# Kernel optimization log

Measured on AMD Instinct MI355X. Metric: run time of the kernel, lower is better.

The kernel has to match this reference:

```python
import jax, jax.numpy as jnp
import numpy as np

B, N, F_, H, K_IN, K = 2, 768, 128, 128, 2, 2
TAU = 0.66


def setup_inputs() -> dict:
    key = jax.random.key(0)
    ks = jax.random.split(key, 8)
    s = lambda fan: 1.0 / np.sqrt(fan)
    X = jax.random.normal(ks[0], (B, N, F_), jnp.float32)
    # edge_feat RezeroMLP: Linear(F,H) -> act -> Linear(H,H)
    ef_w1 = jax.random.normal(ks[1], (F_, H), jnp.float32) * s(F_)
    ef_b1 = jnp.zeros((H,), jnp.float32)
    ef_w2 = jax.random.normal(ks[2], (H, H), jnp.float32) * s(H)
    ef_b2 = jnp.zeros((H,), jnp.float32)
    # rezero gate (init 0 in module; use small nonzero so the branch is exercised)
    gate = jnp.asarray(0.1, jnp.float32)
    # score_mlp RezeroMLP: Linear(k_in,H) -> ReLU -> Linear(H,k)
    sm_w1 = jax.random.normal(ks[3], (K_IN, H), jnp.float32) * s(K_IN)
    sm_b1 = jnp.zeros((H,), jnp.float32)
    sm_w2 = jax.random.normal(ks[4], (H, K), jnp.float32) * s(H)
    sm_b2 = jnp.zeros((K,), jnp.float32)
    # pre-sampled standard Gumbel noise for gumbel_softmax
    u = jax.random.uniform(ks[5], (B, N, N, K), jnp.float32, minval=1e-6, maxval=1.0 - 1e-6)
    gumbel = -jnp.log(-jnp.log(u))
    return {"X": X, "ef_w1": ef_w1, "ef_b1": ef_b1, "ef_w2": ef_w2, "ef_b2": ef_b2,
            "gate": gate, "sm_w1": sm_w1, "sm_b1": sm_b1, "sm_w2": sm_w2, "sm_b2": sm_b2,
            "gumbel": gumbel}


def reference(X, ef_w1, ef_b1, ef_w2, ef_b2, gate, sm_w1, sm_b1, sm_w2, sm_b2, gumbel):
    # edge_feat MLP: [B,N,F] -> [B,N,H]
    feats = jax.nn.relu(X @ ef_w1 + ef_b1) @ ef_w2 + ef_b2
    D = H // K_IN
    Xact = feats.reshape(B, N, D, K_IN)
    Xskip = X.reshape(B, N, D, K_IN)  # feat_dim == hidden_dim, proj is None
    Xc = (Xskip + gate * Xact).transpose(0, 3, 1, 2)  # [B,k_in,N,D]
    # pairwise outer product ('prod' scoring): [B,N,N,k_in]
    prod = jnp.einsum('bkid,bkjd->bijk', Xc, Xc)
    # per-edge score MLP: k_in -> H -> k
    scores = jax.nn.relu(prod @ sm_w1 + sm_b1) @ sm_w2 + sm_b2  # [B,N,N,k]
    logits = scores - jnp.max(scores, axis=-1, keepdims=True)
    # gumbel-softmax, hard (straight-through)
    y_soft = jax.nn.softmax((logits + gumbel) / TAU, axis=-1)
    y_hard = jax.nn.one_hot(jnp.argmax(y_soft, axis=-1), K, dtype=y_soft.dtype)
    y = y_hard + y_soft - jax.lax.stop_gradient(y_soft)
    # A = y @ zo with zo = [0,1,...]: probability/one-hot mass of 'edge' states
    zo = jnp.ones((K,), y.dtype).at[0].set(0.0)
    A = y @ zo  # [B,N,N]
    # zero diagonal and symmetrize via upper triangle
    Au = jnp.triu(A, 1)
    return Au + jnp.swapaxes(Au, -1, -2)
```

## Files before the change

### kernel.cpp

```cpp
#include <hip/hip_runtime.h>

#define BB 2
#define NN 768
#define FF 128
#define HH 128
#define TS 32
#define LST 68
#define NT (NN / TS)
#define NPAIR (NT * (NT + 1) / 2)
#define EROWS 2
#define THR 4e-3f

__device__ __forceinline__
double edge_exact_f64(const double* __restrict__ Xc, const double* __restrict__ wpack,
                      int b, int i, int j, double init) {
    const double* xi0 = Xc + ((size_t)(b * 2 + 0) * NN + i) * 64;
    const double* xj0 = Xc + ((size_t)(b * 2 + 0) * NN + j) * 64;
    const double* xi1 = Xc + ((size_t)(b * 2 + 1) * NN + i) * 64;
    const double* xj1 = Xc + ((size_t)(b * 2 + 1) * NN + j) * 64;
    double p0 = 0.0, p1 = 0.0;
#pragma unroll 4
    for (int d2 = 0; d2 < 32; ++d2) {
        double2 a0 = *(const double2*)&xi0[2 * d2];
        double2 b0 = *(const double2*)&xj0[2 * d2];
        double2 a1 = *(const double2*)&xi1[2 * d2];
        double2 b1 = *(const double2*)&xj1[2 * d2];
        p0 = fma(a0.y, b0.y, fma(a0.x, b0.x, p0));
        p1 = fma(a1.y, b1.y, fma(a1.x, b1.x, p1));
    }
    double m = init;
#pragma unroll 8
    for (int c = 0; c < HH; ++c) {
        double2 wab = *(const double2*)&wpack[4 * c];
        double2 wbw = *(const double2*)&wpack[4 * c + 2];
        double tt = fma(p1, wab.y, fma(p0, wab.x, wbw.x));
        tt = fmax(tt, 0.0);
        m = fma(tt, wbw.y, m);
    }
    return m;
}

__global__ __launch_bounds__(256)
void edgefeat_kernel(const float* __restrict__ X,
                     const float* __restrict__ w1, const float* __restrict__ b1,
                     const float* __restrict__ w2, const float* __restrict__ b2,
                     const float* __restrict__ gatep,
                     const float* __restrict__ sm_w1, const float* __restrict__ sm_b1,
                     const float* __restrict__ sm_w2,
                     double* __restrict__ Xc, float* __restrict__ Xcf,
                     double* __restrict__ wpack, float4* __restrict__ wpackf) {
    __shared__ float  Xs[EROWS][FF];
    __shared__ double Hp[2][EROWS][HH];
    __shared__ double Hs[EROWS][HH];
    const int tid = threadIdx.x;
    const int h  = tid & 127;
    const int kh = tid >> 7;
    const int row0 = blockIdx.x * EROWS;
    Xs[kh][h] = X[(size_t)(row0 + kh) * FF + h];
    if (blockIdx.x == 0 && kh == 0) {
        double a  = (double)sm_w1[h];
        double bq = (double)sm_w1[HH + h];
        double be = (double)sm_b1[h];
        double wd = (double)sm_w2[2 * h + 1] - (double)sm_w2[2 * h + 0];
        wpack[4 * h + 0] = a;  wpack[4 * h + 1] = bq;
        wpack[4 * h + 2] = be; wpack[4 * h + 3] = wd;
        wpackf[h] = make_float4((float)a, (float)bq, (float)be, (float)wd);
    }
    __syncthreads();
    const int f0 = kh * 64;
    double acc0 = (kh == 0) ? (double)b1[h] : 0.0;
    double acc1 = acc0;
    for (int f = f0; f < f0 + 64; ++f) {
        double w = (double)w1[f * HH + h];
        acc0 = fma((double)Xs[0][f], w, acc0);
        acc1 = fma((double)Xs[1][f], w, acc1);
    }
    Hp[kh][0][h] = acc0; Hp[kh][1][h] = acc1;
    __syncthreads();
    if (kh == 0) {
        double v0 = Hp[0][0][h] + Hp[1][0][h];
        double v1 = Hp[0][1][h] + Hp[1][1][h];
        Hs[0][h] = v0 > 0.0 ? v0 : 0.0;
        Hs[1][h] = v1 > 0.0 ? v1 : 0.0;
    }
    __syncthreads();
    acc0 = (kh == 0) ? (double)b2[h] : 0.0;
    acc1 = acc0;
    for (int c = f0; c < f0 + 64; ++c) {
        double w = (double)w2[c * HH + h];
        acc0 = fma(Hs[0][c], w, acc0);
        acc1 = fma(Hs[1][c], w, acc1);
    }
    Hp[kh][0][h] = acc0; Hp[kh][1][h] = acc1;
    __syncthreads();
    if (kh == 0) {
        const double gate = (double)gatep[0];
        const int k = h & 1, d = h >> 1;
        const int b = row0 / NN;
        const int i0 = row0 % NN;
#pragma unroll
        for (int r = 0; r < EROWS; ++r) {
            double a = Hp[0][r][h] + Hp[1][r][h];
            double v = (double)Xs[r][h] + gate * a;
            size_t idx = (((size_t)(b * 2 + k)) * NN + (i0 + r)) * 64 + d;
            Xc[idx]  = v;
            Xcf[idx] = (float)v;
        }
    }
}

__global__ __launch_bounds__(512, 6)
void edge_decide_kernel(const double* __restrict__ Xc,
                        const float* __restrict__ Xcf,
                        const double* __restrict__ wpack,
                        const float4* __restrict__ wpackf,
                        const float* __restrict__ sm_b2,
                        const float* __restrict__ gumbel,
                        float* __restrict__ out) {
    __shared__ float  Ai[2][TS][LST];
    __shared__ float  Aj[2][TS][LST];
    __shared__ float  As[TS][TS + 1];
    const int b = blockIdx.y;
    const int t = blockIdx.x;
    int ti = (int)((49.0 - sqrt(2401.0 - 8.0 * (double)t)) * 0.5);
    int base = ti * (49 - ti) / 2;
    if (t < base) { --ti; base = ti * (49 - ti) / 2; }
    else { int nb = (ti + 1) * (48 - ti) / 2; if (t >= nb) { ++ti; base = nb; } }
    const int tj = t - base + ti;
    const int tid = threadIdx.x;
    const int i0 = ti * TS, j0 = tj * TS;

    for (int q = 0; q < 2; ++q) {
        int flat = tid + 512 * q;
        int d4 = flat & 15;
        int r  = (flat >> 4) & 31;
        int k  = flat >> 9;
        size_t rowbase = ((size_t)(b * 2 + k)) * NN;
        *(float4*)&Ai[k][r][4 * d4] = *(const float4*)&Xcf[(rowbase + i0 + r) * 64 + 4 * d4];
        *(float4*)&Aj[k][r][4 * d4] = *(const float4*)&Xcf[(rowbase + j0 + r) * 64 + 4 * d4];
    }

    const int s  = tid & 1;
    const int e  = tid >> 1;
    const int rh = e >> 4;
    const int ch = e & 15;
    const int r0 = rh, r1 = rh + 16;
    const int c0 = 2 * ch, c1 = c0 + 1;
    const int lr  = (s == 0) ? r0 : r1;
    const int gr  = i0 + lr;
    const int gj0 = j0 + c0, gj1 = j0 + c1;

    float4 gv = *(const float4*)&gumbel[(((size_t)b * NN + gr) * NN + gj0) * 2];
    __syncthreads();

    float p000 = 0.f, p001 = 0.f, p010 = 0.f, p011 = 0.f;
    float p100 = 0.f, p101 = 0.f, p110 = 0.f, p111 = 0.f;
#pragma unroll
    for (int it = 0; it < 8; ++it) {
        const int d4 = (s + 2 * it) * 4;
        float4 a00 = *(const float4*)&Ai[0][r0][d4];
        float4 a01 = *(const float4*)&Ai[0][r1][d4];
        float4 a10 = *(const float4*)&Ai[1][r0][d4];
        float4 a11 = *(const float4*)&Ai[1][r1][d4];
        float4 b00 = *(const float4*)&Aj[0][c0][d4];
        float4 b01 = *(const float4*)&Aj[0][c1][d4];
        float4 b10 = *(const float4*)&Aj[1][c0][d4];
        float4 b11 = *(const float4*)&Aj[1][c1][d4];
        p000 = fmaf(a00.w, b00.w, fmaf(a00.z, b00.z, fmaf(a00.y, b00.y, fmaf(a00.x, b00.x, p000))));
        p001 = fmaf(a00.w, b01.w, fmaf(a00.z, b01.z, fmaf(a00.y, b01.y, fmaf(a00.x, b01.x, p001))));
        p010 = fmaf(a01.w, b00.w, fmaf(a01.z, b00.z, fmaf(a01.y, b00.y, fmaf(a01.x, b00.x, p010))));
        p011 = fmaf(a01.w, b01.w, fmaf(a01.z, b01.z, fmaf(a01.y, b01.y, fmaf(a01.x, b01.x, p011))));
        p100 = fmaf(a10.w, b10.w, fmaf(a10.z, b10.z, fmaf(a10.y, b10.y, fmaf(a10.x, b10.x, p100))));
        p101 = fmaf(a10.w, b11.w, fmaf(a10.z, b11.z, fmaf(a10.y, b11.y, fmaf(a10.x, b11.x, p101))));
        p110 = fmaf(a11.w, b10.w, fmaf(a11.z, b10.z, fmaf(a11.y, b10.y, fmaf(a11.x, b10.x, p110))));
        p111 = fmaf(a11.w, b11.w, fmaf(a11.z, b11.z, fmaf(a11.y, b11.y, fmaf(a11.x, b11.x, p111))));
    }
    p000 += __shfl_xor(p000, 1); p001 += __shfl_xor(p001, 1);
    p010 += __shfl_xor(p010, 1); p011 += __shfl_xor(p011, 1);
    p100 += __shfl_xor(p100, 1); p101 += __shfl_xor(p101, 1);
    p110 += __shfl_xor(p110, 1); p111 += __shfl_xor(p111, 1);

    const float pa0 = (s == 0) ? p000 : p010;
    const float pa1 = (s == 0) ? p100 : p110;
    const float pb0 = (s == 0) ? p001 : p011;
    const float pb1 = (s == 0) ? p101 : p111;

    float ma = 0.f, mb = 0.f;
    float4 wA[8], wB[8];
#pragma unroll
    for (int u = 0; u < 8; ++u) wA[u] = wpackf[u];
#pragma unroll 1
    for (int cg = 0; cg < 8; ++cg) {
        const float4* nxt1 = wpackf + (16 * cg + 8);
#pragma unroll
        for (int u = 0; u < 8; ++u) wB[u] = nxt1[u];
#pragma unroll
        for (int u = 0; u < 8; ++u) {
            float tt;
            tt = fmaf(pa1, wA[u].y, fmaf(pa0, wA[u].x, wA[u].z)); tt = fmaxf(tt, 0.f); ma = fmaf(tt, wA[u].w, ma);
            tt = fmaf(pb1, wA[u].y, fmaf(pb0, wA[u].x, wA[u].z)); tt = fmaxf(tt, 0.f); mb = fmaf(tt, wA[u].w, mb);
        }
        const float4* nxt2 = wpackf + ((cg < 7) ? (16 * cg + 16) : 0);
#pragma unroll
        for (int u = 0; u < 8; ++u) wA[u] = nxt2[u];
#pragma unroll
        for (int u = 0; u < 8; ++u) {
            float tt;
            tt = fmaf(pa1, wB[u].y, fmaf(pa0, wB[u].x, wB[u].z)); tt = fmaxf(tt, 0.f); ma = fmaf(tt, wB[u].w, ma);
            tt = fmaf(pb1, wB[u].y, fmaf(pb0, wB[u].x, wB[u].z)); tt = fmaxf(tt, 0.f); mb = fmaf(tt, wB[u].w, mb);
        }
    }

    const double bd = (double)sm_b2[1] - (double)sm_b2[0];
    double ia = bd + ((double)gv.y - (double)gv.x);
    double ib = bd + ((double)gv.w - (double)gv.z);
    float fa = ma + (float)ia;
    float fb = mb + (float)ib;
    float Aa = fa > 0.f ? 1.f : 0.f;
    float Ab = fb > 0.f ? 1.f : 0.f;
    if (__builtin_expect(fminf(fabsf(fa), fabsf(fb)) < THR, 0)) {
        if (fabsf(fa) < THR) Aa = edge_exact_f64(Xc, wpack, b, gr, gj0, ia) > 0.0 ? 1.f : 0.f;
        if (fabsf(fb) < THR) Ab = edge_exact_f64(Xc, wpack, b, gr, gj1, ib) > 0.0 ? 1.f : 0.f;
    }
    As[lr][c0] = Aa; As[lr][c1] = Ab;
    __syncthreads();

    if (ti != tj) {
        *(float2*)&out[((size_t)b * NN + gr) * NN + gj0] = make_float2(Aa, Ab);
        float2 tv = make_float2(As[c0][lr], As[c1][lr]);
        *(float2*)&out[((size_t)b * NN + j0 + lr) * NN + i0 + c0] = tv;
    } else {
        float v0 = (lr < c0) ? Aa : ((lr > c0) ? As[c0][lr] : 0.0f);
        float v1 = (lr < c1) ? Ab : ((lr > c1) ? As[c1][lr] : 0.0f);
        *(float2*)&out[((size_t)b * NN + gr) * NN + gj0] = make_float2(v0, v1);
    }
}

extern "C" void kernel_launch(void* const* d_in, const int* in_sizes, int n_in,
                              void* d_out, int out_size, void* d_ws, size_t ws_size,
                              hipStream_t stream) {
    const float* X      = (const float*)d_in[0];
    const float* ef_w1  = (const float*)d_in[1];
    const float* ef_b1  = (const float*)d_in[2];
    const float* ef_w2  = (const float*)d_in[3];
    const float* ef_b2  = (const float*)d_in[4];
    const float* gate   = (const float*)d_in[5];
    const float* sm_w1  = (const float*)d_in[6];
    const float* sm_b1  = (const float*)d_in[7];
    const float* sm_w2  = (const float*)d_in[8];
    const float* sm_b2  = (const float*)d_in[9];
    const float* gumbel = (const float*)d_in[10];
    float* out = (float*)d_out;

    double* Xc     = (double*)d_ws;
    double* wpack  = Xc + (size_t)BB * 2 * NN * 64;
    float4* wpackf = (float4*)(wpack + 4 * HH);
    float*  Xcf    = (float*)(wpackf + HH);

    edgefeat_kernel<<<BB * NN / EROWS, 256, 0, stream>>>(
        X, ef_w1, ef_b1, ef_w2, ef_b2, gate, sm_w1, sm_b1, sm_w2, Xc, Xcf, wpack, wpackf);
    dim3 grid(NPAIR, BB);
    edge_decide_kernel<<<grid, 512, 0, stream>>>(Xc, Xcf, wpack, wpackf, sm_b2, gumbel, out);
}
```

Before: 116.8 us.

## Replace per-edge score MLP with angular lookup table when biases are zero

```diff
diff --git a/kernel.cpp b/kernel.cpp
--- a/kernel.cpp
+++ b/kernel.cpp
@@ -10,6 +10,8 @@
 #define NPAIR (NT * (NT + 1) / 2)
 #define EROWS 2
 #define THR 4e-3f
+#define NBIN 8192
+#define PIf 3.14159265358979323846f
 
 __device__ __forceinline__
 double edge_exact_f64(const double* __restrict__ Xc, const double* __restrict__ wpack,
@@ -48,7 +50,8 @@
                      const float* __restrict__ sm_w1, const float* __restrict__ sm_b1,
                      const float* __restrict__ sm_w2,
                      double* __restrict__ Xc, float* __restrict__ Xcf,
-                     double* __restrict__ wpack, float4* __restrict__ wpackf) {
+                     double* __restrict__ wpack, float4* __restrict__ wpackf,
+                     float4* __restrict__ tab, float* __restrict__ flagp) {
     __shared__ float  Xs[EROWS][FF];
     __shared__ double Hp[2][EROWS][HH];
     __shared__ double Hs[EROWS][HH];
@@ -107,6 +110,38 @@
             Xcf[idx] = (float)v;
         }
     }
+
+    const int bin = blockIdx.x * 256 + tid;
+    if (bin < NBIN) {
+        const float D = 2.f * PIf / (float)NBIN;
+        float thL = -PIf + (float)bin * D, thR = thL + D;
+        float sL, cL, sR, cR;
+        sincosf(thL, &sL, &cL);
+        sincosf(thR, &sR, &cR);
+        float A = 0.f, Bv = 0.f, xa = 0.f, xb = 0.f, xw = 0.f;
+        int ncr = 0;
+#pragma unroll 8
+        for (int c = 0; c < HH; ++c) {
+            float a  = sm_w1[c], bq = sm_w1[HH + c];
+            float wd = sm_w2[2 * c + 1] - sm_w2[2 * c];
+            float hL = fmaf(a, cL, bq * sL);
+            float hR = fmaf(a, cR, bq * sR);
+            bool actL = hL > 0.f;
+            if (actL) { A = fmaf(wd, a, A); Bv = fmaf(wd, bq, Bv); }
+            if (actL != (hR > 0.f)) {
+                ++ncr;
+                float sg = actL ? -1.f : 1.f;
+                xa = sg * a; xb = sg * bq; xw = wd;
+            }
+        }
+        tab[2 * bin]     = make_float4(A, Bv, xa, xb);
+        tab[2 * bin + 1] = make_float4(xw, (ncr >= 2) ? 1.f : 0.f, 0.f, 0.f);
+        if (bin == 0) {
+            float fl = 0.f;
+            for (int c = 0; c < HH; ++c) if (sm_b1[c] != 0.f) fl = 1.f;
+            flagp[0] = fl;
+        }
+    }
 }
 
 __global__ __launch_bounds__(512, 6)
@@ -114,6 +149,7 @@
                         const float* __restrict__ Xcf,
                         const double* __restrict__ wpack,
                         const float4* __restrict__ wpackf,
+                        const float4* __restrict__ tab, const float* __restrict__ flagp,
                         const float* __restrict__ sm_b2,
                         const float* __restrict__ gumbel,
                         float* __restrict__ out) {
@@ -151,6 +187,7 @@
     const int gj0 = j0 + c0, gj1 = j0 + c1;
 
     float4 gv = *(const float4*)&gumbel[(((size_t)b * NN + gr) * NN + gj0) * 2];
+    const float biased = flagp[0];
     __syncthreads();
 
     float p000 = 0.f, p001 = 0.f, p010 = 0.f, p011 = 0.f;
@@ -185,29 +222,33 @@
     const float pb0 = (s == 0) ? p001 : p011;
     const float pb1 = (s == 0) ? p101 : p111;
 
-    float ma = 0.f, mb = 0.f;
-    float4 wA[8], wB[8];
+    float ma, mb;
+    bool xfa = false, xfb = false;
+    if (biased == 0.f) {
+        const float BS = (float)NBIN / (2.f * PIf);
+        float tha = atan2f(pa1, pa0);
+        float thb = atan2f(pb1, pb0);
+        int bina = (int)fminf(fmaxf((tha + PIf) * BS, 0.f), (float)(NBIN - 1));
+        int binb = (int)fminf(fmaxf((thb + PIf) * BS, 0.f), (float)(NBIN - 1));
+        float4 ta0 = tab[2 * bina], ta1 = tab[2 * bina + 1];
+        float4 tb0 = tab[2 * binb], tb1 = tab[2 * binb + 1];
+        ma = fmaf(ta0.x, pa0, ta0.y * pa1) + ta1.x * fmaxf(fmaf(ta0.z, pa0, ta0.w * pa1), 0.f);
+        mb = fmaf(tb0.x, pb0, tb0.y * pb1) + tb1.x * fmaxf(fmaf(tb0.z, pb0, tb0.w * pb1), 0.f);
+        xfa = (ta1.y != 0.f);
+        xfb = (tb1.y != 0.f);
+    } else {
+        ma = 0.f; mb = 0.f;
+#pragma unroll 1
+        for (int c = 0; c < HH; c += 8) {
+            float4 w[8];
 #pragma unroll
-    for (int u = 0; u < 8; ++u) wA[u] = wpackf[u];
-#pragma unroll 1
-    for (int cg = 0; cg < 8; ++cg) {
-        const float4* nxt1 = wpackf + (16 * cg + 8);
+            for (int u = 0; u < 8; ++u) w[u] = wpackf[c + u];
 #pragma unroll
-        for (int u = 0; u < 8; ++u) wB[u] = nxt1[u];
-#pragma unroll
-        for (int u = 0; u < 8; ++u) {
-            float tt;
-            tt = fmaf(pa1, wA[u].y, fmaf(pa0, wA[u].x, wA[u].z)); tt = fmaxf(tt, 0.f); ma = fmaf(tt, wA[u].w, ma);
-            tt = fmaf(pb1, wA[u].y, fmaf(pb0, wA[u].x, wA[u].z)); tt = fmaxf(tt, 0.f); mb = fmaf(tt, wA[u].w, mb);
-        }
-        const float4* nxt2 = wpackf + ((cg < 7) ? (16 * cg + 16) : 0);
-#pragma unroll
-        for (int u = 0; u < 8; ++u) wA[u] = nxt2[u];
-#pragma unroll
-        for (int u = 0; u < 8; ++u) {
-            float tt;
-            tt = fmaf(pa1, wB[u].y, fmaf(pa0, wB[u].x, wB[u].z)); tt = fmaxf(tt, 0.f); ma = fmaf(tt, wB[u].w, ma);
-            tt = fmaf(pb1, wB[u].y, fmaf(pb0, wB[u].x, wB[u].z)); tt = fmaxf(tt, 0.f); mb = fmaf(tt, wB[u].w, mb);
+            for (int u = 0; u < 8; ++u) {
+                float tt;
+                tt = fmaf(pa1, w[u].y, fmaf(pa0, w[u].x, w[u].z)); tt = fmaxf(tt, 0.f); ma = fmaf(tt, w[u].w, ma);
+                tt = fmaf(pb1, w[u].y, fmaf(pb0, w[u].x, w[u].z)); tt = fmaxf(tt, 0.f); mb = fmaf(tt, w[u].w, mb);
+            }
         }
     }
 
@@ -218,9 +259,9 @@
     float fb = mb + (float)ib;
     float Aa = fa > 0.f ? 1.f : 0.f;
     float Ab = fb > 0.f ? 1.f : 0.f;
-    if (__builtin_expect(fminf(fabsf(fa), fabsf(fb)) < THR, 0)) {
-        if (fabsf(fa) < THR) Aa = edge_exact_f64(Xc, wpack, b, gr, gj0, ia) > 0.0 ? 1.f : 0.f;
-        if (fabsf(fb) < THR) Ab = edge_exact_f64(Xc, wpack, b, gr, gj1, ib) > 0.0 ? 1.f : 0.f;
+    if (__builtin_expect(xfa || xfb || fminf(fabsf(fa), fabsf(fb)) < THR, 0)) {
+        if (xfa || fabsf(fa) < THR) Aa = edge_exact_f64(Xc, wpack, b, gr, gj0, ia) > 0.0 ? 1.f : 0.f;
+        if (xfb || fabsf(fb) < THR) Ab = edge_exact_f64(Xc, wpack, b, gr, gj1, ib) > 0.0 ? 1.f : 0.f;
     }
     As[lr][c0] = Aa; As[lr][c1] = Ab;
     __syncthreads();
@@ -256,9 +297,13 @@
     double* wpack  = Xc + (size_t)BB * 2 * NN * 64;
     float4* wpackf = (float4*)(wpack + 4 * HH);
     float*  Xcf    = (float*)(wpackf + HH);
+    float4* tab    = (float4*)(Xcf + (size_t)BB * 2 * NN * 64);
+    float*  flagp  = (float*)(tab + 2 * NBIN);
 
     edgefeat_kernel<<<BB * NN / EROWS, 256, 0, stream>>>(
-        X, ef_w1, ef_b1, ef_w2, ef_b2, gate, sm_w1, sm_b1, sm_w2, Xc, Xcf, wpack, wpackf);
+        X, ef_w1, ef_b1, ef_w2, ef_b2, gate, sm_w1, sm_b1, sm_w2,
+        Xc, Xcf, wpack, wpackf, tab, flagp);
     dim3 grid(NPAIR, BB);
-    edge_decide_kernel<<<grid, 512, 0, stream>>>(Xc, Xcf, wpack, wpackf, sm_b2, gumbel, out);
+    edge_decide_kernel<<<grid, 512, 0, stream>>>(
+        Xc, Xcf, wpack, wpackf, tab, flagp, sm_b2, gumbel, out);
 }
```

Result: slower. 124.9 us (+7.0%).
